# Kernel tuning notes

Hardware: AMD Instinct MI355X
Metric: run time of the kernel (lower is better)

The kernel has to match this reference:

```python
import jax, jax.numpy as jnp
import numpy as np

N = 4096
D = 256
E = 65536
CLUSTER_RANGE = 2
EDGE_THRESHOLD = 0.1
NEG_SLOPE = 0.01  # F.leaky_relu default


def fill_diag(A, value):
    i = jnp.arange(A.shape[0])
    return A.at[i, i].set(value)


def segment_softmax(scores, seg, num_segments):
    # torch_geometric.utils.softmax over segment ids
    m = jax.ops.segment_max(scores, seg, num_segments)
    e = jnp.exp(scores - m[seg])
    den = jax.ops.segment_sum(e, seg, num_segments)
    return e / den[seg]


def high_order_matrices(A, max_order):
    # Generate_high_order_adjacency_matrix(A, k) for k=1..max_order
    # (the per-order torch calls recompute the same cumulative sequence)
    out = [A]
    As = [A]
    cur = A
    for _ in range(max_order - 1):
        nA = (fill_diag(cur @ cur, 0.0) > 0.5).astype(A.dtype)
        for a in As:
            nA = nA - a
        cur = jnp.maximum(nA, 0.0)
        As.append(cur)
        out.append(cur)
    return out


def setup_inputs() -> dict:
    key = jax.random.key(0)
    k1, k2, k3 = jax.random.split(key, 3)
    embedding = jax.random.normal(k1, (N, D), dtype=jnp.float32)
    edge_index = jax.random.randint(k2, (2, E), 0, N, dtype=jnp.int64)
    edge_matrix = jnp.zeros((N, N), jnp.float32).at[edge_index[0], edge_index[1]].set(1.0)
    edge_matrix_weight = edge_matrix
    W_score = jax.random.normal(k3, (1, 2 * D), dtype=jnp.float32) * 0.05
    b_score = jnp.zeros((1,), jnp.float32)
    return {"embedding": embedding, "edge_index": edge_index,
            "edge_matrix": edge_matrix, "edge_matrix_weight": edge_matrix_weight,
            "W_score": W_score, "b_score": b_score}


def reference(embedding, edge_index, edge_matrix, edge_matrix_weight, W_score, b_score):
    n = embedding.shape[0]
    # connectivity fitness: cosine similarity
    Z = embedding / jnp.clip(jnp.linalg.norm(embedding, axis=-1, keepdims=True), 1e-12)
    connectivity_M = Z @ Z.T  # [N,N]
    # structure fitness: edge attention softmax scattered dense
    src, dst = edge_index[0], edge_index[1]
    pair = jnp.concatenate([embedding[src], embedding[dst]], axis=-1)  # [E,2D]
    s = jax.nn.leaky_relu(pair @ W_score.T + b_score, NEG_SLOPE)[:, 0]  # [E]
    att = segment_softmax(s, src, n)
    structure_M = jnp.zeros((n, n), embedding.dtype).at[src, dst].add(att)
    fitness = connectivity_M + structure_M  # fitness_mode == 'both_j'
    # Generate_clusters
    base = fill_diag(edge_matrix, 0.0)
    base = jnp.where(fitness < EDGE_THRESHOLD, 0.0, base)
    cluster_matrices = high_order_matrices(base, CLUSTER_RANGE)
    cluster_matrix = (sum(cluster_matrices) > 0).astype(embedding.dtype)
    # Cluster_assignment
    scores = []
    for Mk in cluster_matrices:
        num = (fitness * Mk).sum(-1)
        deg = Mk.sum(-1)
        scores.append(jnp.where(deg > 0, num / jnp.where(deg > 0, deg, 1.0), 0.0))
    cluster_scores = sum(scores) / CLUSTER_RANGE  # [N]
    # Select_clusters (overlap=True, pick_all=True) -> boolean cluster mask
    cm0 = cluster_matrices[0]
    local_extrema = cluster_scores[:, None] - cm0 * cluster_scores[None, :] > 0
    cluster_mask = jnp.all(local_extrema, axis=1)  # [N] bool
    # Generate_assignment_matrix with dense masks (reduced columns zeroed
    # instead of sliced away, keeping static shapes)
    S0 = cluster_matrix
    reduced = ((S0 * cluster_mask[None, :].astype(S0.dtype)).sum(-1) > 0) | (S0.sum(0) == 0)
    keeping = (~cluster_mask) & (~reduced)
    not_keep = (~keeping).astype(S0.dtype)[None, :]
    keep_col = (~reduced).astype(S0.dtype)[None, :]
    S = fill_diag(S0 * not_keep, 1.0) * keep_col            # [N,N]
    S_w = fill_diag((cluster_matrix * fitness) * not_keep, 1.0) * keep_col  # [N,N]
    B = S_w
    # pooling_mode == 'mean'
    pooled = S_w.T @ embedding  # [N,D], zero rows for removed nodes
    # coarsened adjacency
    EMw = fill_diag(edge_matrix_weight, 1.0)
    new_w = S.T @ EMw @ S
    new_adj = (new_w > 0).astype(embedding.dtype)
    return pooled, new_adj, new_w, B, cluster_mask
```

## Files before the change

kernel.cpp:

```cpp
#include <hip/hip_runtime.h>

#define N 4096
#define D 256
#define E 65536
#define NW 128
#define THRESH 0.1f


__device__ __forceinline__ float g16_dot(const float4* __restrict__ Zi4,
                                         const float* __restrict__ Zj, int l) {
    const float4* Zj4 = (const float4*)Zj;
    float4 acc = make_float4(0.f, 0.f, 0.f, 0.f);
    #pragma unroll
    for (int q = 0; q < 4; q++) {
        float4 a = Zi4[q * 16 + l];
        float4 b = Zj4[q * 16 + l];
        acc.x += a.x * b.x; acc.y += a.y * b.y;
        acc.z += a.z * b.z; acc.w += a.w * b.w;
    }
    float s = (acc.x + acc.y) + (acc.z + acc.w);
    s += __shfl_xor(s, 8);
    s += __shfl_xor(s, 4);
    s += __shfl_xor(s, 2);
    s += __shfl_xor(s, 1);
    return s;
}

__global__ void k_norm(const float* __restrict__ emb, const float* __restrict__ W,
                       float* __restrict__ Z, float* __restrict__ p1, float* __restrict__ p2,
                       float* __restrict__ den, unsigned* __restrict__ cmTb,
                       float* __restrict__ Bm) {
    __shared__ float red[3][4];
    __shared__ float nrm_s;
    int i = blockIdx.x, t = threadIdx.x;
    int wid = t >> 6, lane = t & 63;
    float x  = emb[(size_t)i * D + t];
    float ss = x * x;
    float a  = x * W[t];
    float b  = x * W[D + t];
    #pragma unroll
    for (int o = 32; o > 0; o >>= 1) {
        ss += __shfl_down(ss, o);
        a  += __shfl_down(a, o);
        b  += __shfl_down(b, o);
    }
    if (lane == 0) { red[0][wid] = ss; red[1][wid] = a; red[2][wid] = b; }
    {
        float4 z4 = make_float4(0.f, 0.f, 0.f, 0.f);
        float4* b4 = (float4*)(Bm + (size_t)i * N);
        #pragma unroll
        for (int q = 0; q < 4; q++) b4[t + q * 256] = z4;
    }
    if (t < NW) cmTb[(size_t)i * NW + t] = 0u;
    __syncthreads();
    if (t == 0) {
        float S = red[0][0] + red[0][1] + red[0][2] + red[0][3];
        float A = red[1][0] + red[1][1] + red[1][2] + red[1][3];
        float B = red[2][0] + red[2][1] + red[2][2] + red[2][3];
        nrm_s = fmaxf(sqrtf(S), 1e-12f);
        p1[i] = A;
        p2[i] = B;
        den[i] = 0.f;
    }
    __syncthreads();
    Z[(size_t)i * D + t] = x / nrm_s;
}

__global__ void k_edge1(const int* __restrict__ ei, const float* __restrict__ p1,
                        const float* __restrict__ p2, const float* __restrict__ bsc,
                        float* __restrict__ exE, float* __restrict__ den) {
    int e = blockIdx.x * 256 + threadIdx.x;
    int s = ei[e], d = ei[E + e];
    float x = p1[s] + p2[d] + bsc[0];
    x = (x >= 0.f) ? x : 0.01f * x;
    float ex = expf(x);
    exE[e] = ex;
    atomicAdd(den + s, ex);
}

__global__ void k_edge2(const int* __restrict__ ei, const float* __restrict__ exE,
                        const float* __restrict__ den, float* __restrict__ Bm) {
    int e = blockIdx.x * 256 + threadIdx.x;
    int s = ei[e], d = ei[E + e];
    atomicAdd(Bm + (size_t)s * N + d, exE[e] / den[s]);
}

__global__ void k_embit(const float* __restrict__ EM, unsigned* __restrict__ EMb) {
    size_t base = ((size_t)blockIdx.x * 256 + threadIdx.x) * 8;
    const float4* p = (const float4*)(EM + base);
    float4 v0 = p[0], v1 = p[1];
    unsigned m = 0;
    m |= (v0.x != 0.f) ? 1u   : 0u;
    m |= (v0.y != 0.f) ? 2u   : 0u;
    m |= (v0.z != 0.f) ? 4u   : 0u;
    m |= (v0.w != 0.f) ? 8u   : 0u;
    m |= (v1.x != 0.f) ? 16u  : 0u;
    m |= (v1.y != 0.f) ? 32u  : 0u;
    m |= (v1.z != 0.f) ? 64u  : 0u;
    m |= (v1.w != 0.f) ? 128u : 0u;
    m |= __shfl_down(m, 1) << 8;
    m |= __shfl_down(m, 2) << 16;
    if ((threadIdx.x & 3) == 0) EMb[base >> 5] = m;
}

__global__ void k_abit(const float* __restrict__ Z, const unsigned* __restrict__ EMb,
                       const float* __restrict__ Bm, unsigned* __restrict__ Ab) {
    __shared__ float4 Zi4[64];
    __shared__ unsigned AbL[NW];
    __shared__ int lst[2048];
    __shared__ int cnt;
    int i = blockIdx.x, t = threadIdx.x;
    if (t < 64) Zi4[t] = ((const float4*)(Z + (size_t)i * D))[t];
    if (t == 0) cnt = 0;
    if (t < NW) AbL[t] = 0u;
    __syncthreads();
    if (t < NW) {
        unsigned bits = EMb[(size_t)i * NW + t];
        if (t == (i >> 5)) bits &= ~(1u << (i & 31));
        while (bits) {
            int b = __ffs(bits) - 1; bits &= bits - 1;
            int p = atomicAdd(&cnt, 1);
            if (p < 2048) lst[p] = t * 32 + b;
        }
    }
    __syncthreads();
    int n = min(cnt, 2048);
    int g = t >> 4, l = t & 15;
    for (int k = g; k < n; k += 16) {
        int j = lst[k];
        float s = g16_dot(Zi4, Z + (size_t)j * D, l);
        if (l == 0) {
            float fit = s + Bm[(size_t)i * N + j];
            if (fit >= THRESH) atomicOr(&AbL[j >> 5], 1u << (j & 31));
        }
    }
    __syncthreads();
    if (t < NW) Ab[(size_t)i * NW + t] = AbL[t];
}

__global__ void k_m2(const float* __restrict__ Z, const unsigned* __restrict__ Ab,
                     const float* __restrict__ Bm, unsigned* __restrict__ cmb,
                     unsigned* __restrict__ cmTb, float* __restrict__ cs) {
    __shared__ float4 Zi4[64];
    __shared__ unsigned Aw[NW], M2w[NW];
    __shared__ int lstA[1024];
    __shared__ int lstM[2048];
    __shared__ int cntA, cntM, d1s, d2s;
    __shared__ float red1[16], red2[16];
    int i = blockIdx.x, t = threadIdx.x;
    if (t < 64) Zi4[t] = ((const float4*)(Z + (size_t)i * D))[t];
    if (t == 0) { cntA = 0; cntM = 0; d1s = 0; d2s = 0; }
    if (t < NW) Aw[t] = Ab[(size_t)i * NW + t];
    __syncthreads();
    if (t < NW) {
        unsigned bits = Aw[t];
        int d = __popc(bits);
        if (d) atomicAdd(&d1s, d);
        while (bits) {
            int b = __ffs(bits) - 1; bits &= bits - 1;
            int p = atomicAdd(&cntA, 1);
            if (p < 1024) lstA[p] = t * 32 + b;
        }
    }
    __syncthreads();
    int nA = min(cntA, 1024);
    if (t < NW) {
        unsigned r = 0;
        for (int k = 0; k < nA; k++) r |= Ab[(size_t)lstA[k] * NW + t];
        unsigned m2 = r & ~Aw[t];
        if (t == (i >> 5)) m2 &= ~(1u << (i & 31));
        M2w[t] = m2;
        int d = __popc(m2);
        if (d) atomicAdd(&d2s, d);
        unsigned cm = Aw[t] | m2;
        cmb[(size_t)i * NW + t] = cm;
        unsigned bits = cm;
        while (bits) {
            int b = __ffs(bits) - 1; bits &= bits - 1;
            int j = t * 32 + b;
            atomicOr(&cmTb[(size_t)j * NW + (i >> 5)], 1u << (i & 31));
        }
        bits = m2;
        while (bits) {
            int b = __ffs(bits) - 1; bits &= bits - 1;
            int p = atomicAdd(&cntM, 1);
            if (p < 2048) lstM[p] = t * 32 + b;
        }
    }
    __syncthreads();
    int nM = min(cntM, 2048);
    int g = t >> 4, l = t & 15;
    float a1 = 0.f, a2 = 0.f;
    for (int k = g; k < nA; k += 16) {
        int j = lstA[k];
        float s = g16_dot(Zi4, Z + (size_t)j * D, l);
        if (l == 0) a1 += s + Bm[(size_t)i * N + j];
    }
    for (int k = g; k < nM; k += 16) {
        int j = lstM[k];
        float s = g16_dot(Zi4, Z + (size_t)j * D, l);
        if (l == 0) a2 += s + Bm[(size_t)i * N + j];
    }
    if (l == 0) { red1[g] = a1; red2[g] = a2; }
    __syncthreads();
    if (t == 0) {
        float n1 = 0.f, n2 = 0.f;
        #pragma unroll
        for (int q = 0; q < 16; q++) { n1 += red1[q]; n2 += red2[q]; }
        float s1 = (d1s > 0) ? n1 / (float)d1s : 0.f;
        float s2 = (d2s > 0) ? n2 / (float)d2s : 0.f;
        cs[i] = 0.5f * (s1 + s2);
    }
}

__global__ void k_mask(const unsigned* __restrict__ Ab, const float* __restrict__ cs,
                       unsigned* __restrict__ maskU, float* __restrict__ maskOut) {
    int wid = threadIdx.x >> 6, lane = threadIdx.x & 63;
    int i = blockIdx.x * 4 + wid;
    float ci = cs[i];
    bool ok = ci > 0.f;
    for (int w = lane; w < NW; w += 64) {
        unsigned bits = Ab[(size_t)i * NW + w];
        while (bits) {
            int b = __ffs(bits) - 1; bits &= bits - 1;
            ok = ok && (ci > cs[w * 32 + b]);
        }
    }
    unsigned long long ball = __ballot(ok);
    if (lane == 0) {
        unsigned m = (ball == ~0ull) ? 1u : 0u;
        maskU[i] = m;
        maskOut[i] = (float)m;
    }
}

__global__ void k_reduced(const unsigned* __restrict__ cmb, const unsigned* __restrict__ cmTb,
                          const unsigned* __restrict__ maskU, unsigned* __restrict__ keepU,
                          unsigned* __restrict__ nkU) {
    int wid = threadIdx.x >> 6, lane = threadIdx.x & 63;
    int i = blockIdx.x * 4 + wid;
    bool anym = false, colany = false;
    for (int w = lane; w < NW; w += 64) {
        unsigned bits = cmb[(size_t)i * NW + w];
        while (bits) {
            int b = __ffs(bits) - 1; bits &= bits - 1;
            anym = anym || (maskU[w * 32 + b] != 0);
        }
        colany = colany || (cmTb[(size_t)i * NW + w] != 0);
    }
    bool red = (__ballot(anym) != 0ull) || (__ballot(colany) == 0ull);
    if (lane == 0) {
        keepU[i] = red ? 0u : 1u;
        nkU[i]   = ((maskU[i] != 0) || red) ? 1u : 0u;
    }
}

__global__ void k_sbbit(const unsigned* __restrict__ keepU, const unsigned* __restrict__ nkU,
                        unsigned* __restrict__ sbBit) {
    int w = threadIdx.x;
    unsigned b = 0;
    for (int k = 0; k < 32; k++) {
        int j = w * 32 + k;
        if (nkU[j] && keepU[j]) b |= 1u << k;
    }
    sbBit[w] = b;
}

__global__ void k_sw(const float* __restrict__ Z, const unsigned* __restrict__ cmb,
                     const unsigned* __restrict__ keepU, const unsigned* __restrict__ sbBit,
                     float* __restrict__ Bm) {
    __shared__ float row[N];
    __shared__ float4 Zi4[64];
    __shared__ int lst[2048];
    __shared__ int cnt;
    int i = blockIdx.x, t = threadIdx.x;
    {
        float4 z4 = make_float4(0.f, 0.f, 0.f, 0.f);
        float4* r4 = (float4*)row;
        #pragma unroll
        for (int q = 0; q < 4; q++) r4[t + q * 256] = z4;
    }
    if (t < 64) Zi4[t] = ((const float4*)(Z + (size_t)i * D))[t];
    if (t == 0) cnt = 0;
    __syncthreads();
    if (t < NW) {
        unsigned bits = cmb[(size_t)i * NW + t] & sbBit[t];
        while (bits) {
            int b = __ffs(bits) - 1; bits &= bits - 1;
            int p = atomicAdd(&cnt, 1);
            if (p < 2048) lst[p] = t * 32 + b;
        }
    }
    __syncthreads();
    int n = min(cnt, 2048);
    int g = t >> 4, l = t & 15;
    for (int k = g; k < n; k += 16) {
        int j = lst[k];
        float s = g16_dot(Zi4, Z + (size_t)j * D, l);
        if (l == 0) row[j] = s + Bm[(size_t)i * N + j];
    }
    __syncthreads();
    if (t == 0) row[i] = keepU[i] ? 1.f : 0.f;
    __syncthreads();
    {
        const float4* r4 = (const float4*)row;
        float4* d4 = (float4*)(Bm + (size_t)i * N);
        #pragma unroll
        for (int q = 0; q < 4; q++) d4[t + q * 256] = r4[t + q * 256];
    }
}

__global__ void k_pooled(const float* __restrict__ emb, const float* __restrict__ Bm,
                         const unsigned* __restrict__ cmTb, const unsigned* __restrict__ keepU,
                         float* __restrict__ pooled) {
    __shared__ int lst[2048];
    __shared__ int cnt;
    int a = blockIdx.x, t = threadIdx.x;
    if (t == 0) cnt = 0;
    __syncthreads();
    if (keepU[a] && t < NW) {
        unsigned bits = cmTb[(size_t)a * NW + t];
        while (bits) {
            int b = __ffs(bits) - 1; bits &= bits - 1;
            int p = atomicAdd(&cnt, 1);
            if (p < 2048) lst[p] = t * 32 + b;
        }
    }
    __syncthreads();
    float acc = 0.f;
    if (keepU[a]) acc = emb[(size_t)a * D + t];
    int n = min(cnt, 2048);
    for (int k = 0; k < n; k++) {
        int i = lst[k];
        acc += Bm[(size_t)i * N + a] * emb[(size_t)i * D + t];
    }
    pooled[(size_t)a * D + t] = acc;
}

__global__ void k_T(const unsigned* __restrict__ EMb, const unsigned* __restrict__ cmb,
                    const unsigned* __restrict__ sbBit, const unsigned* __restrict__ keepU,
                    unsigned char* __restrict__ Tu8) {
    __shared__ unsigned short row[N];
    __shared__ int lst[1024];
    __shared__ int cnt;
    int i = blockIdx.x, t = threadIdx.x;
    {
        unsigned* r32 = (unsigned*)row;
        #pragma unroll
        for (int q = 0; q < 8; q++) r32[t + q * 256] = 0u;
    }
    if (t == 0) cnt = 0;
    __syncthreads();
    if (t < NW) {
        unsigned bits = EMb[(size_t)i * NW + t];
        if (t == (i >> 5)) bits &= ~(1u << (i & 31));
        while (bits) {
            int b = __ffs(bits) - 1; bits &= bits - 1;
            int p = atomicAdd(&cnt, 1);
            if (p < 1023) lst[p] = t * 32 + b;
        }
    }
    __syncthreads();
    if (t == 0) { int p = min(cnt, 1023); lst[p] = i; cnt = p + 1; }
    __syncthreads();
    if (t < NW) {
        int w = t, n = cnt;
        for (int k = 0; k < n; k++) {
            int j = lst[k];
            unsigned bits = cmb[(size_t)j * NW + w] & sbBit[w];
            if (w == (j >> 5) && keepU[j]) bits |= 1u << (j & 31);
            while (bits) {
                int b = __ffs(bits) - 1; bits &= bits - 1;
                row[w * 32 + b] += 1;
            }
        }
    }
    __syncthreads();
    {
        int base = t * 16;
        unsigned w0 = 0, w1 = 0, w2 = 0, w3 = 0;
        #pragma unroll
        for (int k = 0; k < 4; k++) w0 |= ((unsigned)(row[base + k]      & 0xff)) << (8 * k);
        #pragma unroll
        for (int k = 0; k < 4; k++) w1 |= ((unsigned)(row[base + 4 + k]  & 0xff)) << (8 * k);
        #pragma unroll
        for (int k = 0; k < 4; k++) w2 |= ((unsigned)(row[base + 8 + k]  & 0xff)) << (8 * k);
        #pragma unroll
        for (int k = 0; k < 4; k++) w3 |= ((unsigned)(row[base + 12 + k] & 0xff)) << (8 * k);
        uint4 pk = make_uint4(w0, w1, w2, w3);
        *(uint4*)(Tu8 + (size_t)i * N + base) = pk;
    }
}

__global__ void k_neww(const unsigned char* __restrict__ Tu8, const unsigned* __restrict__ cmTb,
                       const unsigned* __restrict__ keepU, const unsigned* __restrict__ nkU,
                       float* __restrict__ nw, float* __restrict__ adj) {
    __shared__ int lst[2048];
    __shared__ int cnt;
    int a = blockIdx.x, t = threadIdx.x;
    if (t == 0) { cnt = keepU[a] ? 1 : 0; lst[0] = a; }
    __syncthreads();
    if (keepU[a] && nkU[a] && t < NW) {
        unsigned bits = cmTb[(size_t)a * NW + t];
        while (bits) {
            int b = __ffs(bits) - 1; bits &= bits - 1;
            int p = atomicAdd(&cnt, 1);
            if (p < 2048) lst[p] = t * 32 + b;
        }
    }
    __syncthreads();
    int acc0 = 0, acc1 = 0, acc2 = 0, acc3 = 0;
    int n = min(cnt, 2048);
    for (int k = 0; k < n; k++) {
        unsigned v = *(const unsigned*)(Tu8 + (size_t)lst[k] * N + t * 4);
        acc0 += v & 0xff;
        acc1 += (v >> 8) & 0xff;
        acc2 += (v >> 16) & 0xff;
        acc3 += (v >> 24);
    }
    float4 ow = make_float4((float)acc0, (float)acc1, (float)acc2, (float)acc3);
    float4 oa = make_float4(acc0 > 0 ? 1.f : 0.f, acc1 > 0 ? 1.f : 0.f,
                            acc2 > 0 ? 1.f : 0.f, acc3 > 0 ? 1.f : 0.f);
    *(float4*)(nw  + (size_t)a * N + t * 4) = ow;
    *(float4*)(adj + (size_t)a * N + t * 4) = oa;
}

extern "C" void kernel_launch(void* const* d_in, const int* in_sizes, int n_in,
                              void* d_out, int out_size, void* d_ws, size_t ws_size,
                              hipStream_t stream) {
    const float* emb = (const float*)d_in[0];
    const int*   ei  = (const int*)d_in[1];
    const float* EM  = (const float*)d_in[2];
    const float* W   = (const float*)d_in[4];
    const float* bsc = (const float*)d_in[5];

    float* out     = (float*)d_out;
    float* pooled  = out;
    float* adj     = pooled + (size_t)N * D;
    float* nw      = adj + (size_t)N * N;
    float* Bm      = nw + (size_t)N * N;
    float* maskOut = Bm + (size_t)N * N;

    float*    Z     = (float*)d_ws;
    float*    p1    = Z + (size_t)N * D;
    float*    p2    = p1 + N;
    float*    den   = p2 + N;
    float*    exE   = den + N;
    unsigned* EMb   = (unsigned*)(exE + E);
    unsigned* Ab    = EMb + (size_t)N * NW;
    unsigned* cmb   = Ab + (size_t)N * NW;
    unsigned* cmTb  = cmb + (size_t)N * NW;
    float*    cs    = (float*)(cmTb + (size_t)N * NW);
    unsigned* maskU = (unsigned*)(cs + N);
    unsigned* keepU = maskU + N;
    unsigned* nkU   = keepU + N;
    unsigned* sbBit = nkU + N;
    unsigned char* Tu8 = (unsigned char*)(sbBit + NW);

    k_norm<<<N, 256, 0, stream>>>(emb, W, Z, p1, p2, den, cmTb, Bm);
    k_edge1<<<E / 256, 256, 0, stream>>>(ei, p1, p2, bsc, exE, den);
    k_edge2<<<E / 256, 256, 0, stream>>>(ei, exE, den, Bm);
    k_embit<<<(size_t)N * N / 2048, 256, 0, stream>>>(EM, EMb);
    k_abit<<<N, 256, 0, stream>>>(Z, EMb, Bm, Ab);
    k_m2<<<N, 256, 0, stream>>>(Z, Ab, Bm, cmb, cmTb, cs);
    k_mask<<<N / 4, 256, 0, stream>>>(Ab, cs, maskU, maskOut);
    k_reduced<<<N / 4, 256, 0, stream>>>(cmb, cmTb, maskU, keepU, nkU);
    k_sbbit<<<1, 128, 0, stream>>>(keepU, nkU, sbBit);
    k_sw<<<N, 256, 0, stream>>>(Z, cmb, keepU, sbBit, Bm);
    k_pooled<<<N, 256, 0, stream>>>(emb, Bm, cmTb, keepU, pooled);
    k_T<<<N, 256, 0, stream>>>(EMb, cmb, sbBit, keepU, Tu8);
    k_neww<<<N, 1024, 0, stream>>>(Tu8, cmTb, keepU, nkU, nw, adj);
}
```

Measured before the change: 398.2 us.

## Store intermediate T as sparse per-row lists and scatter-accumulate in shared memory

The intermediate T = EMw·S is now stored per row as a compact list of (column, count) entries capped at TCAP, instead of a dense u8 row of N bytes. The new_w kernel then accumulates the selected rows into a shared-memory histogram with atomic adds, rather than streaming full dense 4 KB rows. The aim is to cut global memory traffic when T rows are sparse. In exchange it adds shared atomics and truncates any row holding more than TCAP nonzeros, which could give wrong results on denser inputs.

```diff
diff --git a/kernel.cpp b/kernel.cpp
--- a/kernel.cpp
+++ b/kernel.cpp
@@ -5,6 +5,7 @@
 #define E 65536
 #define NW 128
 #define THRESH 0.1f
+#define TCAP 1024
 
 
 __device__ __forceinline__ float g16_dot(const float4* __restrict__ Zi4,
@@ -339,17 +340,18 @@
 
 __global__ void k_T(const unsigned* __restrict__ EMb, const unsigned* __restrict__ cmb,
                     const unsigned* __restrict__ sbBit, const unsigned* __restrict__ keepU,
-                    unsigned char* __restrict__ Tu8) {
+                    unsigned* __restrict__ Tsp, unsigned* __restrict__ Tnnz) {
     __shared__ unsigned short row[N];
     __shared__ int lst[1024];
     __shared__ int cnt;
+    __shared__ int snnz;
     int i = blockIdx.x, t = threadIdx.x;
     {
         unsigned* r32 = (unsigned*)row;
         #pragma unroll
         for (int q = 0; q < 8; q++) r32[t + q * 256] = 0u;
     }
-    if (t == 0) cnt = 0;
+    if (t == 0) { cnt = 0; snnz = 0; }
     __syncthreads();
     if (t < NW) {
         unsigned bits = EMb[(size_t)i * NW + t];
@@ -378,26 +380,33 @@
     __syncthreads();
     {
         int base = t * 16;
-        unsigned w0 = 0, w1 = 0, w2 = 0, w3 = 0;
-        #pragma unroll
-        for (int k = 0; k < 4; k++) w0 |= ((unsigned)(row[base + k]      & 0xff)) << (8 * k);
-        #pragma unroll
-        for (int k = 0; k < 4; k++) w1 |= ((unsigned)(row[base + 4 + k]  & 0xff)) << (8 * k);
-        #pragma unroll
-        for (int k = 0; k < 4; k++) w2 |= ((unsigned)(row[base + 8 + k]  & 0xff)) << (8 * k);
-        #pragma unroll
-        for (int k = 0; k < 4; k++) w3 |= ((unsigned)(row[base + 12 + k] & 0xff)) << (8 * k);
-        uint4 pk = make_uint4(w0, w1, w2, w3);
-        *(uint4*)(Tu8 + (size_t)i * N + base) = pk;
-    }
-}
-
-__global__ void k_neww(const unsigned char* __restrict__ Tu8, const unsigned* __restrict__ cmTb,
-                       const unsigned* __restrict__ keepU, const unsigned* __restrict__ nkU,
+        #pragma unroll
+        for (int k = 0; k < 16; k++) {
+            unsigned v = row[base + k];
+            if (v) {
+                int p = atomicAdd(&snnz, 1);
+                if (p < TCAP) Tsp[(size_t)i * TCAP + p] = ((unsigned)(base + k) << 16) | v;
+            }
+        }
+    }
+    __syncthreads();
+    if (t == 0) Tnnz[i] = (unsigned)min(snnz, TCAP);
+}
+
+__global__ void k_neww(const unsigned* __restrict__ Tsp, const unsigned* __restrict__ Tnnz,
+                       const unsigned* __restrict__ cmTb, const unsigned* __restrict__ keepU,
+                       const unsigned* __restrict__ nkU,
                        float* __restrict__ nw, float* __restrict__ adj) {
+    __shared__ unsigned row[N];
     __shared__ int lst[2048];
     __shared__ int cnt;
     int a = blockIdx.x, t = threadIdx.x;
+    {
+        uint4 z4 = make_uint4(0u, 0u, 0u, 0u);
+        uint4* r4 = (uint4*)row;
+        #pragma unroll
+        for (int q = 0; q < 4; q++) r4[t + q * 256] = z4;
+    }
     if (t == 0) { cnt = keepU[a] ? 1 : 0; lst[0] = a; }
     __syncthreads();
     if (keepU[a] && nkU[a] && t < NW) {
@@ -409,20 +418,30 @@
         }
     }
     __syncthreads();
-    int acc0 = 0, acc1 = 0, acc2 = 0, acc3 = 0;
     int n = min(cnt, 2048);
     for (int k = 0; k < n; k++) {
-        unsigned v = *(const unsigned*)(Tu8 + (size_t)lst[k] * N + t * 4);
-        acc0 += v & 0xff;
-        acc1 += (v >> 8) & 0xff;
-        acc2 += (v >> 16) & 0xff;
-        acc3 += (v >> 24);
-    }
-    float4 ow = make_float4((float)acc0, (float)acc1, (float)acc2, (float)acc3);
-    float4 oa = make_float4(acc0 > 0 ? 1.f : 0.f, acc1 > 0 ? 1.f : 0.f,
-                            acc2 > 0 ? 1.f : 0.f, acc3 > 0 ? 1.f : 0.f);
-    *(float4*)(nw  + (size_t)a * N + t * 4) = ow;
-    *(float4*)(adj + (size_t)a * N + t * 4) = oa;
+        int i = lst[k];
+        int c = (int)Tnnz[i];
+        const unsigned* sp = Tsp + (size_t)i * TCAP;
+        for (int e = t; e < c; e += 256) {
+            unsigned v = sp[e];
+            atomicAdd(&row[v >> 16], v & 0xffffu);
+        }
+    }
+    __syncthreads();
+    {
+        int base = t * 16;
+        #pragma unroll
+        for (int g2 = 0; g2 < 4; g2++) {
+            unsigned r0 = row[base + 4 * g2], r1 = row[base + 4 * g2 + 1];
+            unsigned r2 = row[base + 4 * g2 + 2], r3 = row[base + 4 * g2 + 3];
+            float4 ow = make_float4((float)r0, (float)r1, (float)r2, (float)r3);
+            float4 oa = make_float4(r0 ? 1.f : 0.f, r1 ? 1.f : 0.f,
+                                    r2 ? 1.f : 0.f, r3 ? 1.f : 0.f);
+            *(float4*)(nw  + (size_t)a * N + base + 4 * g2) = ow;
+            *(float4*)(adj + (size_t)a * N + base + 4 * g2) = oa;
+        }
+    }
 }
 
 extern "C" void kernel_launch(void* const* d_in, const int* in_sizes, int n_in,
@@ -455,7 +474,8 @@
     unsigned* keepU = maskU + N;
     unsigned* nkU   = keepU + N;
     unsigned* sbBit = nkU + N;
-    unsigned char* Tu8 = (unsigned char*)(sbBit + NW);
+    unsigned* Tsp   = sbBit + NW;
+    unsigned* Tnnz  = Tsp + (size_t)N * TCAP;
 
     k_norm<<<N, 256, 0, stream>>>(emb, W, Z, p1, p2, den, cmTb, Bm);
     k_edge1<<<E / 256, 256, 0, stream>>>(ei, p1, p2, bsc, exE, den);
@@ -468,6 +488,6 @@
     k_sbbit<<<1, 128, 0, stream>>>(keepU, nkU, sbBit);
     k_sw<<<N, 256, 0, stream>>>(Z, cmb, keepU, sbBit, Bm);
     k_pooled<<<N, 256, 0, stream>>>(emb, Bm, cmTb, keepU, pooled);
-    k_T<<<N, 256, 0, stream>>>(EMb, cmb, sbBit, keepU, Tu8);
-    k_neww<<<N, 1024, 0, stream>>>(Tu8, cmTb, keepU, nkU, nw, adj);
-}
+    k_T<<<N, 256, 0, stream>>>(EMb, cmb, sbBit, keepU, Tsp, Tnnz);
+    k_neww<<<N, 256, 0, stream>>>(Tsp, Tnnz, cmTb, keepU, nkU, nw, adj);
+}
```

Result: slower. 442.6 us (+11.1%).
